# Optimization experiments

Hardware: AMD Instinct MI355X
Metric: run time of the kernel (lower is better)

Reference implementation:

```python
import jax, jax.numpy as jnp
import numpy as np

N = 80000; E = 1280000; IN = 128; H1 = 128; H2 = 128; H3 = 64
L1D = 512; L2D = 256; OUT = 10; K = 2; GROUP = 40


def setup_inputs() -> dict:
    key = jax.random.key(0)
    ks = jax.random.split(key, 16)
    s = 0.05
    d = {}
    d['x'] = jax.random.normal(ks[0], (N, IN), jnp.float32)
    d['edge_index'] = jax.random.randint(ks[1], (2, E), 0, N, jnp.int32)
    # SGConv linears (applied after K-hop propagation)
    d['W1'] = jax.random.normal(ks[2], (H1, IN), jnp.float32) * s
    d['b1'] = jnp.zeros((H1,), jnp.float32)
    d['W2'] = jax.random.normal(ks[3], (H2, H1), jnp.float32) * s
    d['b2'] = jnp.zeros((H2,), jnp.float32)
    # GATConv (heads=1)
    d['Wg'] = jax.random.normal(ks[4], (H3, H2), jnp.float32) * s
    d['att_src'] = jax.random.normal(ks[5], (H3,), jnp.float32) * s
    d['att_dst'] = jax.random.normal(ks[6], (H3,), jnp.float32) * s
    d['bg'] = jnp.zeros((H3,), jnp.float32)
    # MLP head
    d['L1'] = jax.random.normal(ks[7], (L1D, H3 * GROUP), jnp.float32) * s
    d['bl1'] = jnp.zeros((L1D,), jnp.float32)
    d['L2'] = jax.random.normal(ks[8], (L2D, L1D), jnp.float32) * s
    d['bl2'] = jnp.zeros((L2D,), jnp.float32)
    d['L3'] = jax.random.normal(ks[9], (OUT, L2D), jnp.float32) * s
    d['bl3'] = jnp.zeros((OUT,), jnp.float32)
    return d


def _lrelu(v, slope=0.1):
    return jnp.where(v > 0, v, slope * v)


def _forward(x, src, dst, norm, W1, b1, W2, b2, Wg, bg, att_src, att_dst,
             L1, bl1, L2, bl2, L3, bl3):
    # SGConv: x <- S^K x, then linear. S = D^-1/2 (A+I) D^-1/2
    def prop(h):
        return jax.ops.segment_sum(norm[:, None] * h[src], dst, num_segments=N)

    h = x
    for _ in range(K):
        h = prop(h)
    h = _lrelu(h @ W1.T + b1)
    for _ in range(K):
        h = prop(h)
    h = _lrelu(h @ W2.T + b2)

    # GATConv (1 head), self-loops included in (src, dst)
    g = h @ Wg.T                                   # [N, H3]
    a_s = g @ att_src                              # [N]
    a_d = g @ att_dst                              # [N]
    e = _lrelu(a_s[src] + a_d[dst], 0.2)           # [E+N]
    emax = jax.ops.segment_max(e, dst, num_segments=N)
    ee = jnp.exp(e - emax[dst])
    den = jax.ops.segment_sum(ee, dst, num_segments=N)
    alpha = ee / den[dst]
    h = jax.ops.segment_sum(alpha[:, None] * g[src], dst, num_segments=N) + bg
    h = _lrelu(h)

    # pool 40-node groups, MLP head
    h = h.reshape(N // GROUP, H3 * GROUP)
    h = _lrelu(h @ L1.T + bl1)
    h = _lrelu(h @ L2.T + bl2)
    h = _lrelu(h @ L3.T + bl3)
    return h


def reference(x, edge_index, W1, b1, W2, b2, Wg, bg, att_src, att_dst,
              L1, bl1, L2, bl2, L3, bl3):
    loops = jnp.arange(N, dtype=edge_index.dtype)
    src = jnp.concatenate([edge_index[0], loops])
    dst = jnp.concatenate([edge_index[1], loops])
    deg = jax.ops.segment_sum(jnp.ones_like(src, jnp.float32), dst, num_segments=N)
    dinv = jnp.where(deg > 0, jax.lax.rsqrt(deg), 0.0)
    norm = dinv[src] * dinv[dst]
    return _forward(x, src, dst, norm, W1, b1, W2, b2, Wg, bg, att_src,
                    att_dst, L1, bl1, L2, bl2, L3, bl3)
```

## Files before the change

### kernel.cpp

```cpp
#include <hip/hip_runtime.h>

#define N_NODES 80000
#define N_EDGES 1280000
#define NNZ (N_EDGES + N_NODES)
#define DIM 128
#define HD3 64
#define GROUP 40
#define NPOOL (N_NODES / GROUP)
#define L1DIM 512
#define L2DIM 256
#define OUTD 10
#define SPLITK 4
#define L1K (HD3 * GROUP)

#define SCAN_BLK 1024
#define SCAN_NB ((N_NODES + SCAN_BLK - 1) / SCAN_BLK)

#define NB_BUCKETS ((N_NODES + 255) >> 8)
#define NB_PAD 320
#define EPB 8192
#define NBLK ((NNZ + EPB - 1) / EPB)

typedef unsigned int u32;
typedef unsigned short u16;
typedef __bf16 bf16x8 __attribute__((ext_vector_type(8)));
typedef float f32x4 __attribute__((ext_vector_type(4)));
typedef float f32x2 __attribute__((ext_vector_type(2)));

__device__ __forceinline__ float lrelu(float v, float s) { return v > 0.f ? v : s * v; }

__device__ __forceinline__ float b2f(u16 b) {
    u32 u = ((u32)b) << 16;
    float f; __builtin_memcpy(&f, &u, 4); return f;
}
__device__ __forceinline__ u16 f2b(float f) {
    u32 u; __builtin_memcpy(&u, &f, 4);
    return (u16)((u + 0x7fffu + ((u >> 16) & 1u)) >> 16);
}
__device__ __forceinline__ f32x2 bf2(u32 v) {
    f32x2 r;
    r.x = __uint_as_float(v << 16);
    r.y = __uint_as_float(v & 0xffff0000u);
    return r;
}


__global__ __launch_bounds__(256) void k_hist(const int* __restrict__ ei, u32* __restrict__ cnt) {
    __shared__ u32 h[NB_PAD];
    for (int i = threadIdx.x; i < NB_PAD; i += 256) h[i] = 0;
    __syncthreads();
    int base = blockIdx.x * EPB;
    #pragma unroll 4
    for (int i = 0; i < EPB / 256; ++i) {
        int idx = base + i * 256 + threadIdx.x;
        if (idx < NNZ) {
            int d = (idx < N_EDGES) ? ei[N_EDGES + idx] : idx - N_EDGES;
            atomicAdd(&h[d >> 8], 1u);
        }
    }
    __syncthreads();
    for (int b = threadIdx.x; b < NB_BUCKETS; b += 256)
        cnt[blockIdx.x * NB_PAD + b] = h[b];
}

__global__ __launch_bounds__(256) void k_bscan_col(const u32* __restrict__ cnt,
                                                   u32* __restrict__ basep,
                                                   u32* __restrict__ btot) {
    int b = blockIdx.x, t = threadIdx.x;
    u32 v = (t < NBLK) ? cnt[t * NB_PAD + b] : 0;
    __shared__ u32 sm[256];
    sm[t] = v; __syncthreads();
    for (int off = 1; off < 256; off <<= 1) {
        u32 u = (t >= off) ? sm[t - off] : 0; __syncthreads();
        sm[t] += u; __syncthreads();
    }
    if (t < NBLK) basep[t * NB_PAD + b] = sm[t] - v;
    if (t == 255) btot[b] = sm[255];
}

__global__ __launch_bounds__(512) void k_bscan_top(const u32* __restrict__ btot,
                                                   u32* __restrict__ bbase) {
    __shared__ u32 sm[512];
    int t = threadIdx.x;
    u32 v = (t < NB_BUCKETS) ? btot[t] : 0;
    sm[t] = v; __syncthreads();
    for (int off = 1; off < 512; off <<= 1) {
        u32 u = (t >= off) ? sm[t - off] : 0; __syncthreads();
        sm[t] += u; __syncthreads();
    }
    if (t < NB_BUCKETS) bbase[t] = sm[t] - v;
    if (t == NB_BUCKETS - 1) bbase[NB_BUCKETS] = sm[t];
}

__global__ __launch_bounds__(256) void k_binscatter(const int* __restrict__ ei,
                                                    const u32* __restrict__ basep,
                                                    const u32* __restrict__ bbase,
                                                    uint2* __restrict__ pairs) {
    __shared__ u32 rk[NB_PAD];
    for (int i = threadIdx.x; i < NB_PAD; i += 256) rk[i] = 0;
    __syncthreads();
    int base = blockIdx.x * EPB;
    #pragma unroll 4
    for (int i = 0; i < EPB / 256; ++i) {
        int idx = base + i * 256 + threadIdx.x;
        if (idx < NNZ) {
            int s, d;
            if (idx < N_EDGES) { s = ei[idx]; d = ei[N_EDGES + idx]; }
            else { s = idx - N_EDGES; d = s; }
            int b = d >> 8;
            u32 r = atomicAdd(&rk[b], 1u);
            u32 pos = bbase[b] + basep[blockIdx.x * NB_PAD + b] + r;
            pairs[pos] = make_uint2((u32)s, (u32)d);
        }
    }
}

__global__ __launch_bounds__(256) void k_count2(const uint2* __restrict__ pairs,
                                                const u32* __restrict__ bbase,
                                                int* __restrict__ indeg) {
    __shared__ u32 c[256];
    c[threadIdx.x] = 0;
    __syncthreads();
    int b = blockIdx.x;
    int lo = bbase[b], hi = bbase[b + 1];
    for (int i = lo + threadIdx.x; i < hi; i += 256)
        atomicAdd(&c[pairs[i].y & 255], 1u);
    __syncthreads();
    int node = (b << 8) + threadIdx.x;
    if (node < N_NODES) indeg[node] = (int)c[threadIdx.x];
}

__global__ __launch_bounds__(256) void k_fill2(const uint2* __restrict__ pairs,
                                               const u32* __restrict__ bbase,
                                               const int* __restrict__ row_ptr,
                                               int* __restrict__ col_src) {
    __shared__ u32 c[256];
    c[threadIdx.x] = 0;
    __syncthreads();
    int b = blockIdx.x;
    int lo = bbase[b], hi = bbase[b + 1];
    for (int i = lo + threadIdx.x; i < hi; i += 256) {
        uint2 p = pairs[i];
        u32 r = atomicAdd(&c[p.y & 255], 1u);
        col_src[row_ptr[p.y] + r] = (int)p.x;
    }
}


__global__ __launch_bounds__(256) void k_scan_reduce(const int* __restrict__ indeg,
                                                     int* __restrict__ part) {
    int base = blockIdx.x * SCAN_BLK + threadIdx.x * 4;
    int s = 0;
    if (base < N_NODES) {
        int4 v = *(const int4*)(indeg + base);
        s = v.x + v.y + v.z + v.w;
    }
    for (int off = 32; off; off >>= 1) s += __shfl_xor(s, off);
    __shared__ int sm[4];
    if ((threadIdx.x & 63) == 0) sm[threadIdx.x >> 6] = s;
    __syncthreads();
    if (threadIdx.x == 0) part[blockIdx.x] = sm[0] + sm[1] + sm[2] + sm[3];
}

__global__ __launch_bounds__(128) void k_scan_top(const int* __restrict__ part,
                                                  int* __restrict__ poff,
                                                  int* __restrict__ row_ptr) {
    __shared__ int sm[128];
    int t = threadIdx.x;
    int v = (t < SCAN_NB) ? part[t] : 0;
    sm[t] = v;
    __syncthreads();
    for (int off = 1; off < 128; off <<= 1) {
        int u = (t >= off) ? sm[t - off] : 0;
        __syncthreads();
        sm[t] += u;
        __syncthreads();
    }
    if (t < SCAN_NB) poff[t] = sm[t] - v;
    if (t == 0) row_ptr[N_NODES] = NNZ;
}

__global__ __launch_bounds__(256) void k_scan_apply(const int* __restrict__ indeg,
                                                    const int* __restrict__ poff,
                                                    int* __restrict__ row_ptr,
                                                    float* __restrict__ dinv) {
    int t = threadIdx.x;
    int base = blockIdx.x * SCAN_BLK + t * 4;
    int4 v = {0, 0, 0, 0};
    if (base < N_NODES) v = *(const int4*)(indeg + base);
    int tot = v.x + v.y + v.z + v.w;
    __shared__ int sm[256];
    sm[t] = tot;
    __syncthreads();
    for (int off = 1; off < 256; off <<= 1) {
        int u = (t >= off) ? sm[t - off] : 0;
        __syncthreads();
        sm[t] += u;
        __syncthreads();
    }
    if (base >= N_NODES) return;
    int excl = sm[t] - tot + poff[blockIdx.x];
    int4 p = make_int4(excl, excl + v.x, excl + v.x + v.y, excl + v.x + v.y + v.z);
    *(int4*)(row_ptr + base) = p;
    float4 dv = make_float4(rsqrtf((float)v.x), rsqrtf((float)v.y),
                            rsqrtf((float)v.z), rsqrtf((float)v.w));
    *(float4*)(dinv + base) = dv;
}


__global__ __launch_bounds__(256) void k_f2b(const float* __restrict__ in,
                                             u16* __restrict__ out, int n4) {
    int i = blockIdx.x * blockDim.x + threadIdx.x;
    if (i >= n4) return;
    float4 v = ((const float4*)in)[i];
    ushort4 o = { f2b(v.x), f2b(v.y), f2b(v.z), f2b(v.w) };
    ((ushort4*)out)[i] = o;
}


__global__ __launch_bounds__(256) void k_prop_bf(const int* __restrict__ row_ptr,
                                                 const int* __restrict__ col_src,
                                                 const float* __restrict__ dinv,
                                                 const u16* __restrict__ hin,
                                                 u16* __restrict__ hout) {
    __shared__ float wbuf[4][64];
    int lane = threadIdx.x & 63;
    int wid  = threadIdx.x >> 6;
    int node = blockIdx.x * 4 + wid;
    if (node >= N_NODES) return;
    int j0 = row_ptr[node], j1 = row_ptr[node + 1];
    float dn = dinv[node];
    const int grp = lane >> 4;
    const int dl  = lane & 15;
    f32x2 acc[4] = {};

    for (int base = j0; base < j1; base += 64) {
        int cnt = j1 - base; if (cnt > 64) cnt = 64;
        int jj = base + lane;
        int sidx = 0; float wv = 0.f;
        if (jj < j1) { sidx = col_src[jj]; wv = dinv[sidx] * dn; }
        wbuf[wid][lane] = wv;
        int l = 0;
        for (; l + 16 <= cnt; l += 16) {
            uint4 v[4]; f32x2 w2[4];
            #pragma unroll
            for (int q = 0; q < 4; ++q) {
                int e = l + q * 4 + grp;
                int s = __shfl(sidx, e);
                float wq = wbuf[wid][e];
                w2[q].x = wq; w2[q].y = wq;
                v[q] = *(const uint4*)(hin + (size_t)s * DIM + dl * 8);
            }
            #pragma unroll
            for (int q = 0; q < 4; ++q) {
                acc[0] = __builtin_elementwise_fma(bf2(v[q].x), w2[q], acc[0]);
                acc[1] = __builtin_elementwise_fma(bf2(v[q].y), w2[q], acc[1]);
                acc[2] = __builtin_elementwise_fma(bf2(v[q].z), w2[q], acc[2]);
                acc[3] = __builtin_elementwise_fma(bf2(v[q].w), w2[q], acc[3]);
            }
        }
        for (; l + 4 <= cnt; l += 4) {
            int e = l + grp;
            int s = __shfl(sidx, e);
            float wq = wbuf[wid][e];
            f32x2 w2; w2.x = wq; w2.y = wq;
            uint4 v = *(const uint4*)(hin + (size_t)s * DIM + dl * 8);
            acc[0] = __builtin_elementwise_fma(bf2(v.x), w2, acc[0]);
            acc[1] = __builtin_elementwise_fma(bf2(v.y), w2, acc[1]);
            acc[2] = __builtin_elementwise_fma(bf2(v.z), w2, acc[2]);
            acc[3] = __builtin_elementwise_fma(bf2(v.w), w2, acc[3]);
        }
        for (; l < cnt; ++l) {
            int s = __shfl(sidx, l);
            if (grp == 0) {
                float wq = wbuf[wid][l];
                f32x2 w2; w2.x = wq; w2.y = wq;
                uint4 v = *(const uint4*)(hin + (size_t)s * DIM + dl * 8);
                acc[0] = __builtin_elementwise_fma(bf2(v.x), w2, acc[0]);
                acc[1] = __builtin_elementwise_fma(bf2(v.y), w2, acc[1]);
                acc[2] = __builtin_elementwise_fma(bf2(v.z), w2, acc[2]);
                acc[3] = __builtin_elementwise_fma(bf2(v.w), w2, acc[3]);
            }
        }
    }
    #pragma unroll
    for (int d = 0; d < 4; ++d) {
        acc[d].x += __shfl_xor(acc[d].x, 16); acc[d].x += __shfl_xor(acc[d].x, 32);
        acc[d].y += __shfl_xor(acc[d].y, 16); acc[d].y += __shfl_xor(acc[d].y, 32);
    }
    if (grp == 0) {
        uint4 o;
        o.x = (u32)f2b(acc[0].x) | ((u32)f2b(acc[0].y) << 16);
        o.y = (u32)f2b(acc[1].x) | ((u32)f2b(acc[1].y) << 16);
        o.z = (u32)f2b(acc[2].x) | ((u32)f2b(acc[2].y) << 16);
        o.w = (u32)f2b(acc[3].x) | ((u32)f2b(acc[3].y) << 16);
        *(uint4*)(hout + (size_t)node * DIM + dl * 8) = o;
    }
}


template<int NT, bool BIAS, bool ACT>
__global__ __launch_bounds__(256) void k_gemm_mfma(const u16* __restrict__ A,
                                                   const u16* __restrict__ Wb,
                                                   const float* __restrict__ b,
                                                   u16* __restrict__ C,
                                                   int M, int K) {
    const int lane = threadIdx.x & 63;
    const int wave = threadIdx.x >> 6;
    const int m0 = blockIdx.x * 64 + wave * 16;
    const int row = lane & 15, kg = lane >> 4;
    const int Ntot = NT * 16;

    const u16* Ap = A + (size_t)(m0 + row) * K + kg * 8;
    f32x4 acc[NT] = {};

    for (int k0 = 0; k0 < K; k0 += 32) {
        bf16x8 a = *(const bf16x8*)(Ap + k0);
        #pragma unroll
        for (int nt = 0; nt < NT; ++nt) {
            const u16* Wp = Wb + (size_t)(nt * 16 + row) * K + k0 + kg * 8;
            bf16x8 bb = *(const bf16x8*)Wp;
            acc[nt] = __builtin_amdgcn_mfma_f32_16x16x32_bf16(a, bb, acc[nt], 0, 0, 0);
        }
    }

    #pragma unroll
    for (int nt = 0; nt < NT; ++nt) {
        float bias = BIAS ? b[nt * 16 + row] : 0.f;
        #pragma unroll
        for (int r = 0; r < 4; ++r) {
            float v = acc[nt][r] + bias;
            if (ACT) v = lrelu(v, 0.1f);
            int crow = m0 + kg * 4 + r;
            C[(size_t)crow * Ntot + nt * 16 + row] = f2b(v);
        }
    }
}


template<int NT>
__global__ __launch_bounds__(256) void k_gemm_mfma_sk(const u16* __restrict__ A,
                                                      const u16* __restrict__ Wb,
                                                      float* __restrict__ C,
                                                      int M, int Ntot, int K, int kChunk) {
    const int lane = threadIdx.x & 63;
    const int wave = threadIdx.x >> 6;
    const int m0 = blockIdx.x * 64 + wave * 16;
    const int row = lane & 15, kg = lane >> 4;
    const int n0 = blockIdx.y * NT * 16;
    const int kBeg = blockIdx.z * kChunk;

    int arow = m0 + row; if (arow >= M) arow = M - 1;
    const u16* Ap = A + (size_t)arow * K + kg * 8;
    f32x4 acc[NT] = {};

    for (int k0 = kBeg; k0 < kBeg + kChunk; k0 += 32) {
        bf16x8 a = *(const bf16x8*)(Ap + k0);
        #pragma unroll
        for (int nt = 0; nt < NT; ++nt) {
            const u16* Wp = Wb + (size_t)(n0 + nt * 16 + row) * K + k0 + kg * 8;
            bf16x8 bb = *(const bf16x8*)Wp;
            acc[nt] = __builtin_amdgcn_mfma_f32_16x16x32_bf16(a, bb, acc[nt], 0, 0, 0);
        }
    }

    float* Cp = C + (size_t)blockIdx.z * M * Ntot;
    #pragma unroll
    for (int nt = 0; nt < NT; ++nt) {
        #pragma unroll
        for (int r = 0; r < 4; ++r) {
            int crow = m0 + kg * 4 + r;
            if (crow < M) Cp[(size_t)crow * Ntot + n0 + nt * 16 + row] = acc[nt][r];
        }
    }
}


template<int BM, int BN, int BK, int TM, int TN, bool BIAS, bool ACT>
__global__ __launch_bounds__(256) void k_gemm(const float* __restrict__ A,
                                              const float* __restrict__ W,
                                              const float* __restrict__ b,
                                              float* __restrict__ C,
                                              int M, int Ntot, int K) {
    __shared__ float As[BK][BM + 4];
    __shared__ float Bs[BK][BN + 4];
    const int t = threadIdx.x;
    const int m0 = blockIdx.x * BM, n0 = blockIdx.y * BN;
    const int ty = t / (BN / TN), tx = t % (BN / TN);

    float acc[TM][TN] = {};

    for (int k0 = 0; k0 < K; k0 += BK) {
        #pragma unroll
        for (int p = 0; p < BM * BK / 4 / 256; ++p) {
            int id = p * 256 + t;
            int m = id % BM, kk = (id / BM) * 4;
            float4 v = {0.f, 0.f, 0.f, 0.f};
            if (m0 + m < M) v = *(const float4*)(A + (size_t)(m0 + m) * K + k0 + kk);
            As[kk + 0][m] = v.x; As[kk + 1][m] = v.y;
            As[kk + 2][m] = v.z; As[kk + 3][m] = v.w;
        }
        #pragma unroll
        for (int p = 0; p < BN * BK / 4 / 256; ++p) {
            int id = p * 256 + t;
            int n = id % BN, kk = (id / BN) * 4;
            float4 v = *(const float4*)(W + (size_t)(n0 + n) * K + k0 + kk);
            Bs[kk + 0][n] = v.x; Bs[kk + 1][n] = v.y;
            Bs[kk + 2][n] = v.z; Bs[kk + 3][n] = v.w;
        }
        __syncthreads();

        #pragma unroll
        for (int k = 0; k < BK; ++k) {
            float a[TM], bb[TN];
            #pragma unroll
            for (int i = 0; i < TM; ++i) a[i] = As[k][ty * TM + i];
            #pragma unroll
            for (int j = 0; j < TN; ++j) bb[j] = Bs[k][tx * TN + j];
            #pragma unroll
            for (int i = 0; i < TM; ++i)
                #pragma unroll
                for (int j = 0; j < TN; ++j)
                    acc[i][j] += a[i] * bb[j];
        }
        __syncthreads();
    }

    #pragma unroll
    for (int i = 0; i < TM; ++i) {
        int row = m0 + ty * TM + i;
        if (row >= M) continue;
        float4 o;
        float* op = (float*)&o;
        #pragma unroll
        for (int j = 0; j < TN; ++j) {
            float r = acc[i][j];
            if (BIAS) r += b[n0 + tx * TN + j];
            if (ACT) r = lrelu(r, 0.1f);
            op[j] = r;
        }
        *(float4*)(C + (size_t)row * Ntot + n0 + tx * TN) = o;
    }
}

__global__ __launch_bounds__(256) void k_splitk_reduce(const float* __restrict__ part,
                                                       const float* __restrict__ b,
                                                       float* __restrict__ out) {
    const int total4 = NPOOL * L1DIM / 4;
    int idx = blockIdx.x * blockDim.x + threadIdx.x;
    if (idx >= total4) return;
    const size_t stride4 = (size_t)NPOOL * L1DIM / 4;
    const float4* p4 = (const float4*)part;
    float4 s = p4[idx];
    #pragma unroll
    for (int z = 1; z < SPLITK; ++z) {
        float4 v = p4[idx + z * stride4];
        s.x += v.x; s.y += v.y; s.z += v.z; s.w += v.w;
    }
    int col = (idx * 4) % L1DIM;
    float4 bb = *(const float4*)(b + col);
    s.x = lrelu(s.x + bb.x, 0.1f); s.y = lrelu(s.y + bb.y, 0.1f);
    s.z = lrelu(s.z + bb.z, 0.1f); s.w = lrelu(s.w + bb.w, 0.1f);
    ((float4*)out)[idx] = s;
}


template<int KD, int OD, bool BIAS, bool ACT>
__global__ void k_linear(const float* __restrict__ in, const float* __restrict__ W,
                         const float* __restrict__ b, float* __restrict__ out, int nrows) {
    int idx = blockIdx.x * blockDim.x + threadIdx.x;
    int n = idx / OD, o = idx % OD;
    if (n >= nrows) return;
    const float4* ar = (const float4*)(in + (size_t)n * KD);
    const float4* wr = (const float4*)(W + (size_t)o * KD);
    float4 acc = {0.f, 0.f, 0.f, 0.f};
    #pragma unroll 8
    for (int k = 0; k < KD / 4; ++k) {
        float4 a = ar[k], w = wr[k];
        acc.x += a.x * w.x; acc.y += a.y * w.y;
        acc.z += a.z * w.z; acc.w += a.w * w.w;
    }
    float r = (acc.x + acc.y) + (acc.z + acc.w);
    if (BIAS) r += b[o];
    if (ACT) r = lrelu(r, 0.1f);
    out[idx] = r;
}


__global__ __launch_bounds__(256) void k_attn(const u16* __restrict__ g,
                                              const float* __restrict__ att_src,
                                              const float* __restrict__ att_dst,
                                              float* __restrict__ a_s, float* __restrict__ a_d) {
    int lane = threadIdx.x & 63;
    int node = blockIdx.x * 4 + (threadIdx.x >> 6);
    if (node >= N_NODES) return;
    float v = b2f(g[(size_t)node * HD3 + lane]);
    float s1 = v * att_src[lane];
    float s2 = v * att_dst[lane];
    for (int off = 32; off; off >>= 1) {
        s1 += __shfl_xor(s1, off);
        s2 += __shfl_xor(s2, off);
    }
    if (lane == 0) { a_s[node] = s1; a_d[node] = s2; }
}


__global__ __launch_bounds__(256) void k_gat(const int* __restrict__ row_ptr,
                                             const int* __restrict__ col_src,
                                             const u16* __restrict__ g,
                                             const float* __restrict__ a_s,
                                             const float* __restrict__ a_d,
                                             const float* __restrict__ bg,
                                             u16* __restrict__ hout) {
    __shared__ float wbuf[4][64];
    int lane = threadIdx.x & 63;
    int wid  = threadIdx.x >> 6;
    int node = blockIdx.x * 4 + wid;
    if (node >= N_NODES) return;
    int j0 = row_ptr[node], j1 = row_ptr[node + 1];
    float ad = a_d[node];
    const int grp = lane >> 4, dl = lane & 15;
    float m = -1e30f, den = 0.f;
    f32x2 acc[2] = {};

    for (int base = j0; base < j1; base += 64) {
        int cnt = j1 - base; if (cnt > 64) cnt = 64;
        int jj = base + lane;
        int sidx = 0;
        float e = -1e30f;
        if (jj < j1) { sidx = col_src[jj]; e = lrelu(a_s[sidx] + ad, 0.2f); }
        float cm = e;
        for (int off = 32; off; off >>= 1) cm = fmaxf(cm, __shfl_xor(cm, off));
        float nm = fmaxf(m, cm);
        float scale = __expf(m - nm);
        float wv = (jj < j1) ? __expf(e - nm) : 0.f;
        wbuf[wid][lane] = wv;
        float cden = wv;
        for (int off = 32; off; off >>= 1) cden += __shfl_xor(cden, off);
        den = den * scale + cden;
        f32x2 sc2; sc2.x = scale; sc2.y = scale;
        acc[0] *= sc2; acc[1] *= sc2;
        m = nm;
        int l = 0;
        for (; l + 16 <= cnt; l += 16) {
            uint2 v[4]; f32x2 w2[4];
            #pragma unroll
            for (int q = 0; q < 4; ++q) {
                int e2 = l + q * 4 + grp;
                int s = __shfl(sidx, e2);
                float wq = wbuf[wid][e2];
                w2[q].x = wq; w2[q].y = wq;
                v[q] = *(const uint2*)(g + (size_t)s * HD3 + dl * 4);
            }
            #pragma unroll
            for (int q = 0; q < 4; ++q) {
                acc[0] = __builtin_elementwise_fma(bf2(v[q].x), w2[q], acc[0]);
                acc[1] = __builtin_elementwise_fma(bf2(v[q].y), w2[q], acc[1]);
            }
        }
        for (; l + 4 <= cnt; l += 4) {
            int e2 = l + grp;
            int s = __shfl(sidx, e2);
            float wq = wbuf[wid][e2];
            f32x2 w2; w2.x = wq; w2.y = wq;
            uint2 v = *(const uint2*)(g + (size_t)s * HD3 + dl * 4);
            acc[0] = __builtin_elementwise_fma(bf2(v.x), w2, acc[0]);
            acc[1] = __builtin_elementwise_fma(bf2(v.y), w2, acc[1]);
        }
        for (; l < cnt; ++l) {
            int s = __shfl(sidx, l);
            if (grp == 0) {
                float wq = wbuf[wid][l];
                f32x2 w2; w2.x = wq; w2.y = wq;
                uint2 v = *(const uint2*)(g + (size_t)s * HD3 + dl * 4);
                acc[0] = __builtin_elementwise_fma(bf2(v.x), w2, acc[0]);
                acc[1] = __builtin_elementwise_fma(bf2(v.y), w2, acc[1]);
            }
        }
    }
    #pragma unroll
    for (int d = 0; d < 2; ++d) {
        acc[d].x += __shfl_xor(acc[d].x, 16); acc[d].x += __shfl_xor(acc[d].x, 32);
        acc[d].y += __shfl_xor(acc[d].y, 16); acc[d].y += __shfl_xor(acc[d].y, 32);
    }
    if (grp == 0) {
        float r0 = lrelu(acc[0].x / den + bg[dl * 4 + 0], 0.1f);
        float r1 = lrelu(acc[0].y / den + bg[dl * 4 + 1], 0.1f);
        float r2 = lrelu(acc[1].x / den + bg[dl * 4 + 2], 0.1f);
        float r3 = lrelu(acc[1].y / den + bg[dl * 4 + 3], 0.1f);
        uint2 o;
        o.x = (u32)f2b(r0) | ((u32)f2b(r1) << 16);
        o.y = (u32)f2b(r2) | ((u32)f2b(r3) << 16);
        *(uint2*)(hout + (size_t)node * HD3 + dl * 4) = o;
    }
}


extern "C" void kernel_launch(void* const* d_in, const int* in_sizes, int n_in,
                              void* d_out, int out_size, void* d_ws, size_t ws_size,
                              hipStream_t stream) {
    const float* x   = (const float*)d_in[0];
    const int*   ei  = (const int*)d_in[1];
    const float* W1  = (const float*)d_in[2];
    const float* b1  = (const float*)d_in[3];
    const float* W2  = (const float*)d_in[4];
    const float* b2  = (const float*)d_in[5];
    const float* Wg  = (const float*)d_in[6];
    const float* att_src = (const float*)d_in[7];
    const float* att_dst = (const float*)d_in[8];
    const float* bg  = (const float*)d_in[9];
    const float* L1  = (const float*)d_in[10];
    const float* bl1 = (const float*)d_in[11];
    const float* L2  = (const float*)d_in[12];
    const float* bl2 = (const float*)d_in[13];
    const float* L3  = (const float*)d_in[14];
    const float* bl3 = (const float*)d_in[15];
    float* out = (float*)d_out;

    char* w = (char*)d_ws;
    auto alloc = [&](size_t bytes) {
        char* p = w;
        w += (bytes + 255) & ~(size_t)255;
        return p;
    };
    int*   indeg    = (int*)alloc((size_t)N_NODES * 4);
    int*   row_ptr  = (int*)alloc((size_t)(N_NODES + 1) * 4);
    float* dinv     = (float*)alloc((size_t)N_NODES * 4);
    int*   col_src  = (int*)alloc((size_t)NNZ * 4);
    uint2* pairs    = (uint2*)alloc((size_t)NNZ * 8);
    u32*   cnt      = (u32*)alloc((size_t)NBLK * NB_PAD * 4);
    u32*   basep    = (u32*)alloc((size_t)NBLK * NB_PAD * 4);
    u32*   btot     = (u32*)alloc((size_t)NB_PAD * 4);
    u32*   bbase    = (u32*)alloc((size_t)(NB_BUCKETS + 1) * 4);
    u16*   bufX     = (u16*)alloc((size_t)N_NODES * DIM * 2);
    u16*   bufA     = (u16*)alloc((size_t)N_NODES * DIM * 2);
    u16*   bufB     = (u16*)alloc((size_t)N_NODES * DIM * 2);
    float* a_s      = (float*)alloc((size_t)N_NODES * 4);
    float* a_d      = (float*)alloc((size_t)N_NODES * 4);
    float* p1       = (float*)alloc((size_t)NPOOL * L1DIM * 4);
    float* p2       = (float*)alloc((size_t)NPOOL * L2DIM * 4);
    int*   part     = (int*)alloc((size_t)SCAN_NB * 4);
    int*   poff     = (int*)alloc((size_t)SCAN_NB * 4);
    u16*   W1b      = (u16*)alloc((size_t)DIM * DIM * 2);
    u16*   W2b      = (u16*)alloc((size_t)DIM * DIM * 2);
    u16*   Wgb      = (u16*)alloc((size_t)HD3 * DIM * 2);
    u16*   L1b      = (u16*)alloc((size_t)L1DIM * L1K * 2);
    u16*   gb    = bufX;
    u16*   hGb   = bufA;
    float* skbuf = (float*)bufB;

    dim3 b256(256);
    k_hist<<<NBLK, b256, 0, stream>>>(ei, cnt);
    k_bscan_col<<<NB_BUCKETS, b256, 0, stream>>>(cnt, basep, btot);
    k_bscan_top<<<1, 512, 0, stream>>>(btot, bbase);
    k_binscatter<<<NBLK, b256, 0, stream>>>(ei, basep, bbase, pairs);
    k_count2<<<NB_BUCKETS, b256, 0, stream>>>(pairs, bbase, indeg);
    k_scan_reduce<<<SCAN_NB, b256, 0, stream>>>(indeg, part);
    k_scan_top<<<1, 128, 0, stream>>>(part, poff, row_ptr);
    k_scan_apply<<<SCAN_NB, b256, 0, stream>>>(indeg, poff, row_ptr, dinv);
    k_fill2<<<NB_BUCKETS, b256, 0, stream>>>(pairs, bbase, row_ptr, col_src);

    k_f2b<<<(N_NODES * DIM / 4 + 255) / 256, b256, 0, stream>>>(x, bufX, N_NODES * DIM / 4);
    k_f2b<<<(DIM * DIM / 4 + 255) / 256, b256, 0, stream>>>(W1, W1b, DIM * DIM / 4);
    k_f2b<<<(DIM * DIM / 4 + 255) / 256, b256, 0, stream>>>(W2, W2b, DIM * DIM / 4);
    k_f2b<<<(HD3 * DIM / 4 + 255) / 256, b256, 0, stream>>>(Wg, Wgb, HD3 * DIM / 4);
    k_f2b<<<(L1DIM * L1K / 4 + 255) / 256, b256, 0, stream>>>(L1, L1b, L1DIM * L1K / 4);

    int nb = (N_NODES + 3) / 4;
    int gemm_nb = N_NODES / 64;
    k_prop_bf<<<nb, b256, 0, stream>>>(row_ptr, col_src, dinv, bufX, bufA);
    k_prop_bf<<<nb, b256, 0, stream>>>(row_ptr, col_src, dinv, bufA, bufB);
    k_gemm_mfma<8, true, true><<<gemm_nb, b256, 0, stream>>>(bufB, W1b, b1, bufA, N_NODES, DIM);
    k_prop_bf<<<nb, b256, 0, stream>>>(row_ptr, col_src, dinv, bufA, bufB);
    k_prop_bf<<<nb, b256, 0, stream>>>(row_ptr, col_src, dinv, bufB, bufA);
    k_gemm_mfma<8, true, true><<<gemm_nb, b256, 0, stream>>>(bufA, W2b, b2, bufB, N_NODES, DIM);
    k_gemm_mfma<4, false, false><<<gemm_nb, b256, 0, stream>>>(bufB, Wgb, nullptr, gb, N_NODES, DIM);
    k_attn<<<nb, b256, 0, stream>>>(gb, att_src, att_dst, a_s, a_d);
    k_gat<<<nb, b256, 0, stream>>>(row_ptr, col_src, gb, a_s, a_d, bg, hGb);
    k_gemm_mfma_sk<8><<<dim3(32, 4, SPLITK), b256, 0, stream>>>(
        hGb, L1b, skbuf, NPOOL, L1DIM, L1K, L1K / SPLITK);
    k_splitk_reduce<<<(NPOOL * L1DIM / 4 + 255) / 256, b256, 0, stream>>>(skbuf, bl1, p1);
    k_gemm<64, 64, 32, 4, 4, true, true><<<dim3(32, 4), b256, 0, stream>>>(p1, L2, bl2, p2, NPOOL, L2DIM, L1DIM);
    k_linear<256, 10, true, true><<<(NPOOL * 10 + 255) / 256, b256, 0, stream>>>(p2, L3, bl3, out, NPOOL);
}
```

Before: 511.8 us.

## Pack edge pairs into 32 bits, fuse bf16 conversions, drop LDS weight buffer

Edge pairs are now packed into a single u32: the source index sits in the low 24 bits and the destination's low 8 bits in the high 8, with the bucket id supplying the rest. This halves the pairs buffer traffic in scatter, count and fill. The five float-to-bf16 conversion launches are merged into one kernel that picks its source and destination by index range. In propagation, the shared-memory weight buffer is removed and each lane computes dinv[s]*dn at use time. That adds a gather from dinv per edge in exchange for dropping LDS stores and loads.

```diff
diff --git a/kernel.cpp b/kernel.cpp
--- a/kernel.cpp
+++ b/kernel.cpp
@@ -21,6 +21,13 @@
 #define EPB 8192
 #define NBLK ((NNZ + EPB - 1) / EPB)
 
+#define QX  (N_NODES * DIM / 4)
+#define QW1 (DIM * DIM / 4)
+#define QW2 (DIM * DIM / 4)
+#define QWG (HD3 * DIM / 4)
+#define QL1 (L1DIM * L1K / 4)
+#define QTOT (QX + QW1 + QW2 + QWG + QL1)
+
 typedef unsigned int u32;
 typedef unsigned short u16;
 typedef __bf16 bf16x8 __attribute__((ext_vector_type(8)));
@@ -95,7 +102,7 @@
 __global__ __launch_bounds__(256) void k_binscatter(const int* __restrict__ ei,
                                                     const u32* __restrict__ basep,
                                                     const u32* __restrict__ bbase,
-                                                    uint2* __restrict__ pairs) {
+                                                    u32* __restrict__ pairs) {
     __shared__ u32 rk[NB_PAD];
     for (int i = threadIdx.x; i < NB_PAD; i += 256) rk[i] = 0;
     __syncthreads();
@@ -110,12 +117,12 @@
             int b = d >> 8;
             u32 r = atomicAdd(&rk[b], 1u);
             u32 pos = bbase[b] + basep[blockIdx.x * NB_PAD + b] + r;
-            pairs[pos] = make_uint2((u32)s, (u32)d);
-        }
-    }
-}
-
-__global__ __launch_bounds__(256) void k_count2(const uint2* __restrict__ pairs,
+            pairs[pos] = ((u32)(d & 255) << 24) | (u32)s;
+        }
+    }
+}
+
+__global__ __launch_bounds__(256) void k_count2(const u32* __restrict__ pairs,
                                                 const u32* __restrict__ bbase,
                                                 int* __restrict__ indeg) {
     __shared__ u32 c[256];
@@ -124,13 +131,13 @@
     int b = blockIdx.x;
     int lo = bbase[b], hi = bbase[b + 1];
     for (int i = lo + threadIdx.x; i < hi; i += 256)
-        atomicAdd(&c[pairs[i].y & 255], 1u);
+        atomicAdd(&c[pairs[i] >> 24], 1u);
     __syncthreads();
     int node = (b << 8) + threadIdx.x;
     if (node < N_NODES) indeg[node] = (int)c[threadIdx.x];
 }
 
-__global__ __launch_bounds__(256) void k_fill2(const uint2* __restrict__ pairs,
+__global__ __launch_bounds__(256) void k_fill2(const u32* __restrict__ pairs,
                                                const u32* __restrict__ bbase,
                                                const int* __restrict__ row_ptr,
                                                int* __restrict__ col_src) {
@@ -140,9 +147,11 @@
     int b = blockIdx.x;
     int lo = bbase[b], hi = bbase[b + 1];
     for (int i = lo + threadIdx.x; i < hi; i += 256) {
-        uint2 p = pairs[i];
-        u32 r = atomicAdd(&c[p.y & 255], 1u);
-        col_src[row_ptr[p.y] + r] = (int)p.x;
+        u32 p = pairs[i];
+        u32 dl = p >> 24;
+        int dst = (b << 8) + (int)dl;
+        u32 r = atomicAdd(&c[dl], 1u);
+        col_src[row_ptr[dst] + r] = (int)(p & 0xFFFFFFu);
     }
 }
 
@@ -208,13 +217,22 @@
 }
 
 
-__global__ __launch_bounds__(256) void k_f2b(const float* __restrict__ in,
-                                             u16* __restrict__ out, int n4) {
+__global__ __launch_bounds__(256) void k_f2b_all(const float* __restrict__ x,   u16* __restrict__ xb,
+                                                 const float* __restrict__ w1,  u16* __restrict__ w1b,
+                                                 const float* __restrict__ w2,  u16* __restrict__ w2b,
+                                                 const float* __restrict__ wg,  u16* __restrict__ wgb,
+                                                 const float* __restrict__ l1,  u16* __restrict__ l1b) {
     int i = blockIdx.x * blockDim.x + threadIdx.x;
-    if (i >= n4) return;
-    float4 v = ((const float4*)in)[i];
+    const float* src; u16* dst; int off;
+    if (i < QX)                      { src = x;  dst = xb;  off = i; }
+    else if (i < QX + QW1)           { src = w1; dst = w1b; off = i - QX; }
+    else if (i < QX + QW1 + QW2)     { src = w2; dst = w2b; off = i - QX - QW1; }
+    else if (i < QX + QW1 + QW2 + QWG) { src = wg; dst = wgb; off = i - QX - QW1 - QW2; }
+    else if (i < QTOT)               { src = l1; dst = l1b; off = i - QX - QW1 - QW2 - QWG; }
+    else return;
+    float4 v = ((const float4*)src)[off];
     ushort4 o = { f2b(v.x), f2b(v.y), f2b(v.z), f2b(v.w) };
-    ((ushort4*)out)[i] = o;
+    ((ushort4*)dst)[off] = o;
 }
 
 
@@ -223,10 +241,8 @@
                                                  const float* __restrict__ dinv,
                                                  const u16* __restrict__ hin,
                                                  u16* __restrict__ hout) {
-    __shared__ float wbuf[4][64];
     int lane = threadIdx.x & 63;
-    int wid  = threadIdx.x >> 6;
-    int node = blockIdx.x * 4 + wid;
+    int node = blockIdx.x * 4 + (threadIdx.x >> 6);
     if (node >= N_NODES) return;
     int j0 = row_ptr[node], j1 = row_ptr[node + 1];
     float dn = dinv[node];
@@ -237,17 +253,14 @@
     for (int base = j0; base < j1; base += 64) {
         int cnt = j1 - base; if (cnt > 64) cnt = 64;
         int jj = base + lane;
-        int sidx = 0; float wv = 0.f;
-        if (jj < j1) { sidx = col_src[jj]; wv = dinv[sidx] * dn; }
-        wbuf[wid][lane] = wv;
+        int sidx = (jj < j1) ? col_src[jj] : 0;
         int l = 0;
         for (; l + 16 <= cnt; l += 16) {
             uint4 v[4]; f32x2 w2[4];
             #pragma unroll
             for (int q = 0; q < 4; ++q) {
-                int e = l + q * 4 + grp;
-                int s = __shfl(sidx, e);
-                float wq = wbuf[wid][e];
+                int s = __shfl(sidx, l + q * 4 + grp);
+                float wq = dinv[s] * dn;
                 w2[q].x = wq; w2[q].y = wq;
                 v[q] = *(const uint4*)(hin + (size_t)s * DIM + dl * 8);
             }
@@ -260,9 +273,8 @@
             }
         }
         for (; l + 4 <= cnt; l += 4) {
-            int e = l + grp;
-            int s = __shfl(sidx, e);
-            float wq = wbuf[wid][e];
+            int s = __shfl(sidx, l + grp);
+            float wq = dinv[s] * dn;
             f32x2 w2; w2.x = wq; w2.y = wq;
             uint4 v = *(const uint4*)(hin + (size_t)s * DIM + dl * 8);
             acc[0] = __builtin_elementwise_fma(bf2(v.x), w2, acc[0]);
@@ -273,7 +285,7 @@
         for (; l < cnt; ++l) {
             int s = __shfl(sidx, l);
             if (grp == 0) {
-                float wq = wbuf[wid][l];
+                float wq = dinv[s] * dn;
                 f32x2 w2; w2.x = wq; w2.y = wq;
                 uint4 v = *(const uint4*)(hin + (size_t)s * DIM + dl * 8);
                 acc[0] = __builtin_elementwise_fma(bf2(v.x), w2, acc[0]);
@@ -627,7 +639,7 @@
     int*   row_ptr  = (int*)alloc((size_t)(N_NODES + 1) * 4);
     float* dinv     = (float*)alloc((size_t)N_NODES * 4);
     int*   col_src  = (int*)alloc((size_t)NNZ * 4);
-    uint2* pairs    = (uint2*)alloc((size_t)NNZ * 8);
+    u32*   pairs    = (u32*)alloc((size_t)NNZ * 4);
     u32*   cnt      = (u32*)alloc((size_t)NBLK * NB_PAD * 4);
     u32*   basep    = (u32*)alloc((size_t)NBLK * NB_PAD * 4);
     u32*   btot     = (u32*)alloc((size_t)NB_PAD * 4);
@@ -660,11 +672,7 @@
     k_scan_apply<<<SCAN_NB, b256, 0, stream>>>(indeg, poff, row_ptr, dinv);
     k_fill2<<<NB_BUCKETS, b256, 0, stream>>>(pairs, bbase, row_ptr, col_src);
 
-    k_f2b<<<(N_NODES * DIM / 4 + 255) / 256, b256, 0, stream>>>(x, bufX, N_NODES * DIM / 4);
-    k_f2b<<<(DIM * DIM / 4 + 255) / 256, b256, 0, stream>>>(W1, W1b, DIM * DIM / 4);
-    k_f2b<<<(DIM * DIM / 4 + 255) / 256, b256, 0, stream>>>(W2, W2b, DIM * DIM / 4);
-    k_f2b<<<(HD3 * DIM / 4 + 255) / 256, b256, 0, stream>>>(Wg, Wgb, HD3 * DIM / 4);
-    k_f2b<<<(L1DIM * L1K / 4 + 255) / 256, b256, 0, stream>>>(L1, L1b, L1DIM * L1K / 4);
+    k_f2b_all<<<(QTOT + 255) / 256, b256, 0, stream>>>(x, bufX, W1, W1b, W2, W2b, Wg, Wgb, L1, L1b);
 
     int nb = (N_NODES + 3) / 4;
     int gemm_nb = N_NODES / 64;
```

After: 491.5 us. 1.04x faster.
